# Kernel tuning notes

Hardware: AMD Instinct MI355X
Metric: run time of the kernel (lower is better)

Reference implementation:

```python
import jax, jax.numpy as jnp
import numpy as np

NUM_HEADS = 16


def setup_inputs() -> dict:
    key = jax.random.key(0)
    ks = jax.random.split(key, 5)
    B, L, D = 2, 2048, 1024
    x = jax.random.normal(ks[0], (B, L, D), dtype=jnp.float32)
    s = 1.0 / np.sqrt(D)
    Wqkv_w = jax.random.normal(ks[1], (3 * D, D), dtype=jnp.float32) * s
    Wqkv_b = jax.random.normal(ks[2], (3 * D,), dtype=jnp.float32) * 0.01
    out_w = jax.random.normal(ks[3], (D, D), dtype=jnp.float32) * s
    out_b = jax.random.normal(ks[4], (D,), dtype=jnp.float32) * 0.01
    return {"x": x, "Wqkv_w": Wqkv_w, "Wqkv_b": Wqkv_b, "out_w": out_w, "out_b": out_b}


def reference(x, Wqkv_w, Wqkv_b, out_w, out_b):
    B, L, D = x.shape
    H = NUM_HEADS
    d = D // H
    scale = 1.0 / np.sqrt(d).astype(np.float32)
    # qkv projection: torch Linear is x @ W^T + b
    qkv = x @ Wqkv_w.T + Wqkv_b                      # [B, L, 3D]
    qkv = qkv.reshape(B, L, 3, H, d)                 # (three h d) split
    qkv = jnp.transpose(qkv, (2, 0, 3, 1, 4))        # [3, B, H, L, d]
    q, k, v = qkv[0], qkv[1], qkv[2]
    k = k * scale
    # Linear-attention recurrence S_t = S_{t-1} + v_t k_t^T, y_t = S_t q_t
    # == causally-masked unnormalized attention: y_t = sum_{s<=t} (q_t.k_s) v_s
    scores = jnp.einsum('bhld,bhmd->bhlm', q, k)     # [B,H,L,L]
    causal = jnp.tril(jnp.ones((L, L), dtype=scores.dtype))
    y = jnp.einsum('bhlm,bhmd->bhld', scores * causal, v)  # [B,H,L,d]
    y = jnp.transpose(y, (0, 2, 1, 3)).reshape(B, L, D)    # b l (h d)
    return y @ out_w.T + out_b
```

## Files before the change

kernel.cpp:

```cpp
#include <hip/hip_runtime.h>


#define DEV __device__ __forceinline__

typedef __attribute__((ext_vector_type(8))) short bf16x8;
typedef __attribute__((ext_vector_type(4))) float f32x4;

DEV ushort f2bf(float f) {
  union { float f; unsigned u; } v; v.f = f;
  unsigned r = v.u + 0x7fffu + ((v.u >> 16) & 1u);
  return (ushort)(r >> 16);
}
DEV float bf2f(unsigned b) {
  union { unsigned u; float f; } v; v.u = (b & 0xffffu) << 16;
  return v.f;
}
DEV void glds16(const ushort* g, ushort* l) {
  __builtin_amdgcn_global_load_lds(
      (const __attribute__((address_space(1))) unsigned int*)g,
      (__attribute__((address_space(3))) unsigned int*)l, 16, 0, 0);
}

__global__ __launch_bounds__(256) void cvt_all(const float* __restrict__ x,
                                               const float* __restrict__ Ww,
                                               const float* __restrict__ Ow,
                                               ushort* __restrict__ xb,
                                               ushort* __restrict__ wqkvb,
                                               ushort* __restrict__ outwb) {
  int i = blockIdx.x * 256 + threadIdx.x;
  const float* src; ushort* dst; int off;
  if (i < 1048576)      { src = x;  dst = xb;    off = i; }
  else if (i < 1835008) { src = Ww; dst = wqkvb; off = i - 1048576; }
  else                  { src = Ow; dst = outwb; off = i - 1835008; }
  float4 v = ((const float4*)src)[off];
  ushort4 o;
  o.x = f2bf(v.x); o.y = f2bf(v.y); o.z = f2bf(v.z); o.w = f2bf(v.w);
  ((ushort4*)dst)[off] = o;
}

template <bool OUT_BF16, bool KSCALE>
__global__ __launch_bounds__(256) void gemm_bt(const ushort* __restrict__ A,
                                               const ushort* __restrict__ Bw,
                                               const float* __restrict__ bias,
                                               void* __restrict__ Cout,
                                               int M, int N, int K) {
  __shared__ ushort As[128 * 32];
  __shared__ ushort Bs[128 * 32];
  const int t = threadIdx.x;
  const int wid = t >> 6, lane = t & 63;
  const int quad = lane >> 4, l16 = lane & 15;
  const int bm = blockIdx.y * 128, bn = blockIdx.x * 128;
  const int wm = (wid >> 1) * 64, wn = (wid & 1) * 64;

  f32x4 acc[4][4];
  const f32x4 z = {0.f, 0.f, 0.f, 0.f};
#pragma unroll
  for (int i = 0; i < 4; ++i)
#pragma unroll
    for (int j = 0; j < 4; ++j) acc[i][j] = z;

  const ushort* ag = A + (size_t)(bm + (t >> 2)) * K + ((t & 3) * 8);
  const ushort* bg = Bw + (size_t)(bn + (t >> 2)) * K + ((t & 3) * 8);
  ushort* asl = As + wid * 512;
  ushort* bsl = Bs + wid * 512;
  const size_t rowskip = (size_t)64 * K;

  for (int k0 = 0; k0 < K; k0 += 32) {
    glds16(ag + k0, asl);
    glds16(ag + k0 + rowskip, asl + 2048);
    glds16(bg + k0, bsl);
    glds16(bg + k0 + rowskip, bsl + 2048);
    __syncthreads();
    bf16x8 af[4], bf[4];
#pragma unroll
    for (int i = 0; i < 4; ++i) {
      af[i] = *(const bf16x8*)(As + (wm + i * 16 + l16) * 32 + quad * 8);
      bf[i] = *(const bf16x8*)(Bs + (wn + i * 16 + l16) * 32 + quad * 8);
    }
#pragma unroll
    for (int i = 0; i < 4; ++i)
#pragma unroll
      for (int j = 0; j < 4; ++j)
        acc[i][j] = __builtin_amdgcn_mfma_f32_16x16x32_bf16(af[i], bf[j], acc[i][j], 0, 0, 0);
    __syncthreads();
  }

#pragma unroll
  for (int i = 0; i < 4; ++i)
#pragma unroll
    for (int j = 0; j < 4; ++j) {
      const int col = bn + wn + j * 16 + l16;
      const float bv = bias[col];
      float sc = 1.f;
      if (KSCALE) sc = ((col >> 10) == 1) ? 0.125f : 1.f;
#pragma unroll
      for (int r = 0; r < 4; ++r) {
        const int row = bm + wm + i * 16 + quad * 4 + r;
        const float v = (acc[i][j][r] + bv) * sc;
        if (OUT_BF16)
          ((ushort*)Cout)[(size_t)row * N + col] = f2bf(v);
        else
          ((float*)Cout)[(size_t)row * N + col] = v;
      }
    }
}

__global__ __launch_bounds__(256) void gemm_out64(const ushort* __restrict__ A,
                                                  const ushort* __restrict__ Bw,
                                                  const float* __restrict__ bias,
                                                  float* __restrict__ C,
                                                  int M, int N, int K) {
  __shared__ ushort As[64 * 32];
  __shared__ ushort Bs[128 * 32];
  const int t = threadIdx.x;
  const int wid = t >> 6, lane = t & 63;
  const int quad = lane >> 4, l16 = lane & 15;
  const int bm = blockIdx.y * 64, bn = blockIdx.x * 128;
  const int wn = wid * 32;

  f32x4 acc[4][2];
  const f32x4 z = {0.f, 0.f, 0.f, 0.f};
#pragma unroll
  for (int i = 0; i < 4; ++i) { acc[i][0] = z; acc[i][1] = z; }

  const ushort* ag = A + (size_t)(bm + (t >> 2)) * K + ((t & 3) * 8);
  const ushort* bg = Bw + (size_t)(bn + (t >> 2)) * K + ((t & 3) * 8);
  ushort* asl = As + wid * 512;
  ushort* bsl = Bs + wid * 512;
  const size_t rowskip = (size_t)64 * K;

  for (int k0 = 0; k0 < K; k0 += 32) {
    glds16(ag + k0, asl);
    glds16(bg + k0, bsl);
    glds16(bg + k0 + rowskip, bsl + 2048);
    __syncthreads();
    bf16x8 af[4], bf[2];
#pragma unroll
    for (int i = 0; i < 4; ++i)
      af[i] = *(const bf16x8*)(As + (i * 16 + l16) * 32 + quad * 8);
#pragma unroll
    for (int j = 0; j < 2; ++j)
      bf[j] = *(const bf16x8*)(Bs + (wn + j * 16 + l16) * 32 + quad * 8);
#pragma unroll
    for (int i = 0; i < 4; ++i)
#pragma unroll
      for (int j = 0; j < 2; ++j)
        acc[i][j] = __builtin_amdgcn_mfma_f32_16x16x32_bf16(af[i], bf[j], acc[i][j], 0, 0, 0);
    __syncthreads();
  }

#pragma unroll
  for (int i = 0; i < 4; ++i)
#pragma unroll
    for (int j = 0; j < 2; ++j) {
      const int col = bn + wn + j * 16 + l16;
      const float bv = bias[col];
#pragma unroll
      for (int r = 0; r < 4; ++r) {
        const int row = bm + i * 16 + quad * 4 + r;
        C[(size_t)row * N + col] = acc[i][j][r] + bv;
      }
    }
}

__global__ __launch_bounds__(256) void kv_local(const ushort* __restrict__ qkv,
                                                float* __restrict__ mlocT) {
  const int c = blockIdx.x, bh = blockIdx.y;
  const int b = bh >> 4, hd = bh & 15;
  const int t = threadIdx.x;
  const int wid = t >> 6, lane = t & 63;
  const int quad = lane >> 4, l16 = lane & 15;
  __shared__ ushort kT[64 * 136];
  __shared__ ushort vT[64 * 136];

  {
    const int row = t & 127;
    const int isv = t >> 7;
    const ushort* g = qkv + (size_t)(b * 2048 + c * 128 + row) * 3072 +
                      1024 + isv * 1024 + hd * 64;
    ushort tmp[64];
#pragma unroll
    for (int q = 0; q < 8; ++q) *(uint4*)(tmp + q * 8) = *(const uint4*)(g + q * 8);
    ushort* dst = isv ? vT : kT;
#pragma unroll
    for (int j = 0; j < 64; ++j) dst[j * 136 + row] = tmp[j];
  }
  __syncthreads();

  const f32x4 z = {0.f, 0.f, 0.f, 0.f};
  f32x4 acc[4];
#pragma unroll
  for (int ct = 0; ct < 4; ++ct) acc[ct] = z;
#pragma unroll
  for (int kc = 0; kc < 4; ++kc) {
    bf16x8 afr = *(const bf16x8*)(vT + (wid * 16 + l16) * 136 + kc * 32 + quad * 8);
#pragma unroll
    for (int ct = 0; ct < 4; ++ct) {
      bf16x8 bfr = *(const bf16x8*)(kT + (ct * 16 + l16) * 136 + kc * 32 + quad * 8);
      acc[ct] = __builtin_amdgcn_mfma_f32_16x16x32_bf16(afr, bfr, acc[ct], 0, 0, 0);
    }
  }

  float* outp = mlocT + ((size_t)bh * 16 + c) * 4096;
#pragma unroll
  for (int ct = 0; ct < 4; ++ct)
#pragma unroll
    for (int r = 0; r < 4; ++r)
      outp[(wid * 16 + quad * 4 + r) * 64 + ct * 16 + l16] = acc[ct][r];
}

__global__ __launch_bounds__(256) void kv_prefix(const float* __restrict__ mlocT,
                                                 ushort* __restrict__ statesT) {
  const int slice = blockIdx.x, bh = blockIdx.y;
  const int eidx = slice * 256 + threadIdx.x;
  float run = 0.f;
  for (int c = 0; c < 16; ++c) {
    const size_t idx = ((size_t)bh * 16 + c) * 4096 + eidx;
    statesT[idx] = f2bf(run);
    run += mlocT[idx];
  }
}

__global__ __launch_bounds__(256) void attn_chunk(const ushort* __restrict__ qkv,
                                                  const ushort* __restrict__ statesT,
                                                  ushort* __restrict__ yb) {
  const int c = blockIdx.x, bh = blockIdx.y;
  const int b = bh >> 4, hd = bh & 15;
  const int l0 = c * 128;
  const int t = threadIdx.x;
  const int wid = t >> 6, lane = t & 63;
  const int quad = lane >> 4, l16 = lane & 15;

  __shared__ ushort P[16384];
  __shared__ ushort U[16384];
  ushort* Qs = U;
  ushort* Ks = U + 8192;
  ushort* vT = U;
  ushort* sT = U + 8704;

  {
    uint4 zz; zz.x = zz.y = zz.z = zz.w = 0u;
    uint4* p4 = (uint4*)P;
#pragma unroll
    for (int i = 0; i < 8; ++i) p4[i * 256 + t] = zz;
  }
  {
    const int kcs = ((lane & 7) ^ (lane >> 3)) * 8;
    const ushort* qg = qkv + (size_t)(b * 2048 + l0 + (t >> 3)) * 3072 + hd * 64 + kcs;
    ushort* ql = Qs + wid * 512;
    ushort* kl = Ks + wid * 512;
#pragma unroll
    for (int h2 = 0; h2 < 4; ++h2) {
      glds16(qg + (size_t)h2 * 32 * 3072, ql + h2 * 2048);
      glds16(qg + (size_t)h2 * 32 * 3072 + 1024, kl + h2 * 2048);
    }
  }
  __syncthreads();

  bf16x8 qf[2][2];
#pragma unroll
  for (int i = 0; i < 2; ++i)
#pragma unroll
    for (int kc = 0; kc < 2; ++kc)
      qf[i][kc] = *(const bf16x8*)(Qs + ((wid * 2 + i) * 16 + l16) * 64 +
                                   (((kc * 4 + quad) ^ (l16 & 7)) * 8));

  const f32x4 z4 = {0.f, 0.f, 0.f, 0.f};
  f32x4 pacc[2][8];
#pragma unroll
  for (int i = 0; i < 2; ++i)
#pragma unroll
    for (int j = 0; j < 8; ++j) pacc[i][j] = z4;

#pragma unroll
  for (int i = 0; i < 2; ++i) {
    const int rt = wid * 2 + i;
#pragma unroll
    for (int tj = 0; tj < 8; ++tj) {
      if (tj <= rt) {
#pragma unroll
        for (int kc = 0; kc < 2; ++kc) {
          bf16x8 kfr = *(const bf16x8*)(Ks + (tj * 16 + l16) * 64 +
                                        (((kc * 4 + quad) ^ (l16 & 7)) * 8));
          pacc[i][tj] = __builtin_amdgcn_mfma_f32_16x16x32_bf16(qf[i][kc], kfr, pacc[i][tj], 0, 0, 0);
        }
      }
    }
  }
  __syncthreads();

#pragma unroll
  for (int i = 0; i < 2; ++i) {
    const int rt = wid * 2 + i;
#pragma unroll
    for (int tj = 0; tj < 8; ++tj) {
      if (tj <= rt) {
#pragma unroll
        for (int r = 0; r < 4; ++r) {
          const int row = rt * 16 + quad * 4 + r;
          const int scol = tj * 16 + l16;
          const float v = (scol <= row) ? pacc[i][tj][r] : 0.f;
          P[row * 128 + (((scol >> 3) ^ (row & 7)) * 8) + (scol & 7)] = f2bf(v);
        }
      }
    }
  }
  {
    const int sstep = t >> 1, eb = (t & 1) * 32;
    const ushort* vg = qkv + (size_t)(b * 2048 + l0 + sstep) * 3072 + 2048 + hd * 64 + eb;
    ushort tmp[32];
    *(uint4*)(tmp + 0)  = *(const uint4*)(vg + 0);
    *(uint4*)(tmp + 8)  = *(const uint4*)(vg + 8);
    *(uint4*)(tmp + 16) = *(const uint4*)(vg + 16);
    *(uint4*)(tmp + 24) = *(const uint4*)(vg + 24);
#pragma unroll
    for (int j = 0; j < 32; ++j) vT[(eb + j) * 136 + sstep] = tmp[j];
  }
  {
    const ushort* sg = statesT + ((size_t)bh * 16 + c) * 4096;
#pragma unroll
    for (int h = 0; h < 2; ++h) {
      const int cc = h * 256 + t;
      uint4 d = *(const uint4*)(sg + cc * 8);
      *(uint4*)(sT + (cc >> 3) * 72 + (cc & 7) * 8) = d;
    }
  }
  __syncthreads();

  f32x4 yacc[2][4];
#pragma unroll
  for (int i = 0; i < 2; ++i)
#pragma unroll
    for (int j = 0; j < 4; ++j) yacc[i][j] = z4;

#pragma unroll
  for (int i = 0; i < 2; ++i) {
    const int rt = wid * 2 + i;
    const int kcmax = rt >> 1;
#pragma unroll
    for (int kc = 0; kc < 4; ++kc) {
      if (kc <= kcmax) {
        const int prow = rt * 16 + l16;
        bf16x8 pf;
        *(uint4*)&pf = *(const uint4*)(P + prow * 128 + (((kc * 4 + quad) ^ (prow & 7)) * 8));
#pragma unroll
        for (int ct = 0; ct < 4; ++ct) {
          bf16x8 vf = *(const bf16x8*)(vT + (ct * 16 + l16) * 136 + kc * 32 + quad * 8);
          yacc[i][ct] = __builtin_amdgcn_mfma_f32_16x16x32_bf16(pf, vf, yacc[i][ct], 0, 0, 0);
        }
      }
    }
#pragma unroll
    for (int kc = 0; kc < 2; ++kc) {
#pragma unroll
      for (int ct = 0; ct < 4; ++ct) {
        bf16x8 sf = *(const bf16x8*)(sT + (ct * 16 + l16) * 72 + kc * 32 + quad * 8);
        yacc[i][ct] = __builtin_amdgcn_mfma_f32_16x16x32_bf16(qf[i][kc], sf, yacc[i][ct], 0, 0, 0);
      }
    }
  }

#pragma unroll
  for (int i = 0; i < 2; ++i) {
    const int rt = wid * 2 + i;
#pragma unroll
    for (int ct = 0; ct < 4; ++ct) {
#pragma unroll
      for (int r = 0; r < 4; ++r) {
        const int row = rt * 16 + quad * 4 + r;
        const int e = ct * 16 + l16;
        yb[(size_t)(b * 2048 + l0 + row) * 1024 + hd * 64 + e] = f2bf(yacc[i][ct][r]);
      }
    }
  }
}

extern "C" void kernel_launch(void* const* d_in, const int* in_sizes, int n_in,
                              void* d_out, int out_size, void* d_ws, size_t ws_size,
                              hipStream_t stream) {
  const float* x  = (const float*)d_in[0];
  const float* Ww = (const float*)d_in[1];
  const float* Wb = (const float*)d_in[2];
  const float* Ow = (const float*)d_in[3];
  const float* Ob = (const float*)d_in[4];
  float* out = (float*)d_out;

  char* ws = (char*)d_ws;
  ushort* xb      = (ushort*)(ws);
  ushort* wqkvb   = (ushort*)(ws + (size_t)8  * 1024 * 1024);
  ushort* outwb   = (ushort*)(ws + (size_t)14 * 1024 * 1024);
  ushort* qkvb    = (ushort*)(ws + (size_t)16 * 1024 * 1024);
  float*  mlocT   = (float*) (ws + (size_t)40 * 1024 * 1024);
  ushort* statesT = (ushort*)(ws + (size_t)48 * 1024 * 1024);
  ushort* yb      = (ushort*)(ws + (size_t)52 * 1024 * 1024);

  cvt_all<<<8192, 256, 0, stream>>>(x, Ww, Ow, xb, wqkvb, outwb);
  gemm_bt<true, true><<<dim3(24, 32), 256, 0, stream>>>(xb, wqkvb, Wb, (void*)qkvb, 4096, 3072, 1024);
  kv_local<<<dim3(16, 32), 256, 0, stream>>>(qkvb, mlocT);
  kv_prefix<<<dim3(16, 32), 256, 0, stream>>>(mlocT, statesT);
  attn_chunk<<<dim3(16, 32), 256, 0, stream>>>(qkvb, statesT, yb);
  gemm_out64<<<dim3(8, 64), 256, 0, stream>>>(yb, outwb, Ob, out, 4096, 1024, 1024);
}
```

Before: 162.7 us.

## Replace QKV GEMM with 256x256 double-buffered 8-wave pipelined kernel

Replaces the simple 128x128, BK=32 QKV projection GEMM with a 256x256-tile, BK=64 kernel running 8 waves. It double-buffers LDS with XOR-swizzled layout, interleaves async global-to-LDS loads between MFMA phases, uses setprio and explicit waitcnt control, and remaps blocks so neighbouring ones share data in cache. The aim is to hide memory latency, cut LDS bank conflicts and raise MFMA utilisation. In exchange it launches only 192 blocks, which may underfill the 256 CUs, and it uses large register and LDS budgets.

```diff
diff --git a/kernel.cpp b/kernel.cpp
--- a/kernel.cpp
+++ b/kernel.cpp
@@ -38,69 +38,114 @@
   ((ushort4*)dst)[off] = o;
 }
 
-template <bool OUT_BF16, bool KSCALE>
-__global__ __launch_bounds__(256) void gemm_bt(const ushort* __restrict__ A,
-                                               const ushort* __restrict__ Bw,
-                                               const float* __restrict__ bias,
-                                               void* __restrict__ Cout,
-                                               int M, int N, int K) {
-  __shared__ ushort As[128 * 32];
-  __shared__ ushort Bs[128 * 32];
+__global__ __launch_bounds__(512, 2) void gemm_8p(const ushort* __restrict__ A,
+                                                  const ushort* __restrict__ Bw,
+                                                  const float* __restrict__ bias,
+                                                  ushort* __restrict__ Cout) {
+  __shared__ __align__(16) ushort As[2][2][8192];
+  __shared__ __align__(16) ushort Bs[2][2][8192];
   const int t = threadIdx.x;
-  const int wid = t >> 6, lane = t & 63;
+  const int lane = t & 63, wid = t >> 6;
   const int quad = lane >> 4, l16 = lane & 15;
-  const int bm = blockIdx.y * 128, bn = blockIdx.x * 128;
-  const int wm = (wid >> 1) * 64, wn = (wid & 1) * 64;
-
-  f32x4 acc[4][4];
+  const int wm2 = wid >> 2, wn4 = wid & 3;
+  const int K = 1024, N = 3072;
+
+  const int bid = blockIdx.x;
+  const int wg = (bid & 7) * 24 + (bid >> 3);
+  const int bx = wg % 12, by = wg / 12;
+  const int bm = by << 8, bn = bx << 8;
+
+  const int scol = ((t & 7) ^ ((t >> 3) & 7)) << 3;
+  const ushort* ag = A + (size_t)(bm + (t >> 3)) * K + scol;
+  const ushort* bg = Bw + (size_t)(bn + (t >> 3)) * K + scol;
+
+  f32x4 acc[8][4];
   const f32x4 z = {0.f, 0.f, 0.f, 0.f};
 #pragma unroll
-  for (int i = 0; i < 4; ++i)
+  for (int i = 0; i < 8; ++i)
 #pragma unroll
     for (int j = 0; j < 4; ++j) acc[i][j] = z;
 
-  const ushort* ag = A + (size_t)(bm + (t >> 2)) * K + ((t & 3) * 8);
-  const ushort* bg = Bw + (size_t)(bn + (t >> 2)) * K + ((t & 3) * 8);
-  ushort* asl = As + wid * 512;
-  ushort* bsl = Bs + wid * 512;
-  const size_t rowskip = (size_t)64 * K;
-
-  for (int k0 = 0; k0 < K; k0 += 32) {
-    glds16(ag + k0, asl);
-    glds16(ag + k0 + rowskip, asl + 2048);
-    glds16(bg + k0, bsl);
-    glds16(bg + k0 + rowskip, bsl + 2048);
-    __syncthreads();
-    bf16x8 af[4], bf[4];
-#pragma unroll
-    for (int i = 0; i < 4; ++i) {
-      af[i] = *(const bf16x8*)(As + (wm + i * 16 + l16) * 32 + quad * 8);
-      bf[i] = *(const bf16x8*)(Bs + (wn + i * 16 + l16) * 32 + quad * 8);
-    }
-#pragma unroll
-    for (int i = 0; i < 4; ++i)
-#pragma unroll
-      for (int j = 0; j < 4; ++j)
-        acc[i][j] = __builtin_amdgcn_mfma_f32_16x16x32_bf16(af[i], bf[j], acc[i][j], 0, 0, 0);
-    __syncthreads();
-  }
-
-#pragma unroll
-  for (int i = 0; i < 4; ++i)
-#pragma unroll
-    for (int j = 0; j < 4; ++j) {
-      const int col = bn + wn + j * 16 + l16;
+  const int cx8 = l16 & 7;
+
+#define SG_A(bi, h, kt) \
+  glds16(ag + (size_t)((h)*128) * K + ((kt) << 6), &As[bi][h][wid * 512]); \
+  glds16(ag + (size_t)((h)*128 + 64) * K + ((kt) << 6), &As[bi][h][4096 + wid * 512])
+#define SG_B(bi, h, kt) \
+  glds16(bg + (size_t)((h)*128) * K + ((kt) << 6), &Bs[bi][h][wid * 512]); \
+  glds16(bg + (size_t)((h)*128 + 64) * K + ((kt) << 6), &Bs[bi][h][4096 + wid * 512])
+#define RD_A(bi, mi, kc) \
+  (*(const bf16x8*)&As[bi][(mi) >> 2][(wm2 * 64 + ((mi)&3) * 16 + l16) * 64 + \
+                                      ((((kc)*4 + quad) ^ cx8) << 3)])
+#define RD_B(bi, nj, kc) \
+  (*(const bf16x8*)&Bs[bi][wn4 >> 1][((wn4 & 1) * 64 + (nj)*16 + l16) * 64 + \
+                                     ((((kc)*4 + quad) ^ cx8) << 3)])
+
+  bf16x8 bfr[4][2];
+
+#define PHASE(rbuf, m0, m1, STAGE_STMT, LAST) do { \
+    bf16x8 pa00 = RD_A(rbuf, m0, 0), pa01 = RD_A(rbuf, m0, 1); \
+    bf16x8 pa10 = RD_A(rbuf, m1, 0), pa11 = RD_A(rbuf, m1, 1); \
+    STAGE_STMT; \
+    __builtin_amdgcn_s_barrier(); \
+    asm volatile("s_waitcnt lgkmcnt(0)" ::: "memory"); \
+    __builtin_amdgcn_s_setprio(1); \
+    _Pragma("unroll") \
+    for (int nj = 0; nj < 4; ++nj) { \
+      acc[m0][nj] = __builtin_amdgcn_mfma_f32_16x16x32_bf16(pa00, bfr[nj][0], acc[m0][nj], 0, 0, 0); \
+      acc[m0][nj] = __builtin_amdgcn_mfma_f32_16x16x32_bf16(pa01, bfr[nj][1], acc[m0][nj], 0, 0, 0); \
+      acc[m1][nj] = __builtin_amdgcn_mfma_f32_16x16x32_bf16(pa10, bfr[nj][0], acc[m1][nj], 0, 0, 0); \
+      acc[m1][nj] = __builtin_amdgcn_mfma_f32_16x16x32_bf16(pa11, bfr[nj][1], acc[m1][nj], 0, 0, 0); \
+    } \
+    __builtin_amdgcn_s_setprio(0); \
+    if (!(LAST)) __builtin_amdgcn_s_barrier(); \
+  } while (0)
+
+#define GROUP(rbuf, kt) do { \
+    _Pragma("unroll") \
+    for (int nj = 0; nj < 4; ++nj) { \
+      bfr[nj][0] = RD_B(rbuf, nj, 0); \
+      bfr[nj][1] = RD_B(rbuf, nj, 1); \
+    } \
+    PHASE(rbuf, 0, 1, if ((kt) + 1 < 16) { SG_A(1 - (rbuf), 1, (kt) + 1); }, 0); \
+    PHASE(rbuf, 2, 3, if ((kt) + 2 < 16) { SG_B(rbuf, 0, (kt) + 2); }, 0); \
+    PHASE(rbuf, 4, 5, if ((kt) + 2 < 16) { SG_B(rbuf, 1, (kt) + 2); }, 0); \
+    PHASE(rbuf, 6, 7, if ((kt) + 2 < 16) { SG_A(rbuf, 0, (kt) + 2); }, 1); \
+    if ((kt) < 15) { \
+      if ((kt) == 14) asm volatile("s_waitcnt vmcnt(0)" ::: "memory"); \
+      else            asm volatile("s_waitcnt vmcnt(6)" ::: "memory"); \
+      __builtin_amdgcn_s_barrier(); \
+    } \
+  } while (0)
+
+  SG_B(0, 0, 0); SG_B(0, 1, 0); SG_A(0, 0, 0); SG_A(0, 1, 0);
+  SG_B(1, 0, 1); SG_B(1, 1, 1); SG_A(1, 0, 1);
+  asm volatile("s_waitcnt vmcnt(6)" ::: "memory");
+  __builtin_amdgcn_s_barrier();
+
+  for (int kt2 = 0; kt2 < 16; kt2 += 2) {
+    GROUP(0, kt2);
+    GROUP(1, kt2 + 1);
+  }
+
+#undef GROUP
+#undef PHASE
+#undef RD_A
+#undef RD_B
+#undef SG_A
+#undef SG_B
+
+#pragma unroll
+  for (int mi = 0; mi < 8; ++mi)
+#pragma unroll
+    for (int nj = 0; nj < 4; ++nj) {
+      const int col = bn + wn4 * 64 + nj * 16 + l16;
       const float bv = bias[col];
-      float sc = 1.f;
-      if (KSCALE) sc = ((col >> 10) == 1) ? 0.125f : 1.f;
+      const float sc = ((col >> 10) == 1) ? 0.125f : 1.f;
 #pragma unroll
       for (int r = 0; r < 4; ++r) {
-        const int row = bm + wm + i * 16 + quad * 4 + r;
-        const float v = (acc[i][j][r] + bv) * sc;
-        if (OUT_BF16)
-          ((ushort*)Cout)[(size_t)row * N + col] = f2bf(v);
-        else
-          ((float*)Cout)[(size_t)row * N + col] = v;
+        const int row = bm + (mi >> 2) * 128 + wm2 * 64 + (mi & 3) * 16 + quad * 4 + r;
+        Cout[(size_t)row * N + col] = f2bf((acc[mi][nj][r] + bv) * sc);
       }
     }
 }
@@ -395,7 +440,7 @@
   ushort* yb      = (ushort*)(ws + (size_t)52 * 1024 * 1024);
 
   cvt_all<<<8192, 256, 0, stream>>>(x, Ww, Ow, xb, wqkvb, outwb);
-  gemm_bt<true, true><<<dim3(24, 32), 256, 0, stream>>>(xb, wqkvb, Wb, (void*)qkvb, 4096, 3072, 1024);
+  gemm_8p<<<dim3(192), 512, 0, stream>>>(xb, wqkvb, Wb, qkvb);
   kv_local<<<dim3(16, 32), 256, 0, stream>>>(qkvb, mlocT);
   kv_prefix<<<dim3(16, 32), 256, 0, stream>>>(mlocT, statesT);
   attn_chunk<<<dim3(16, 32), 256, 0, stream>>>(qkvb, statesT, yb);
```

New measurement: 161.6 us. Within noise of the previous version (-0.7%).
